# Optimization experiments

Measured on AMD Instinct MI355X. Metric: run time of the kernel, lower is better.

## Reference

```python
import jax, jax.numpy as jnp
import numpy as np

NUM_HEADS = 12
LOCAL_RATIO = 0.1


def setup_inputs() -> dict:
    key = jax.random.key(0)
    ks = jax.random.split(key, 8)
    B, N, C = 64, 785, 768
    x = jax.random.normal(ks[0], (B, N, C), dtype=jnp.float32)
    attention_rollout = jax.random.uniform(ks[1], (B, N, N), dtype=jnp.float32)
    s = 1.0 / np.sqrt(C)
    # Linear weights stored as [in, out] so y = x @ W + b (torch stores transposed)
    Wq = jax.random.normal(ks[2], (C, C), dtype=jnp.float32) * s
    bq = jax.random.normal(ks[3], (C,), dtype=jnp.float32) * 0.01
    Wkv = jax.random.normal(ks[4], (C, 2 * C), dtype=jnp.float32) * s
    bkv = jax.random.normal(ks[5], (2 * C,), dtype=jnp.float32) * 0.01
    Wp = jax.random.normal(ks[6], (C, C), dtype=jnp.float32) * s
    bp = jax.random.normal(ks[7], (C,), dtype=jnp.float32) * 0.01
    return {"x": x, "attention_rollout": attention_rollout, "Wq": Wq, "bq": bq,
            "Wkv": Wkv, "bkv": bkv, "Wp": Wp, "bp": bp}


def reference(x, attention_rollout, Wq, bq, Wkv, bkv, Wp, bp):
    B, N, C = x.shape
    H = NUM_HEADS
    D = C // H
    scale = D ** -0.5
    num_local = max(1, int(LOCAL_RATIO * (N - 1)))  # static

    # --- top-R% query selection from attention rollout (CLS row, skip CLS col) ---
    cls_attention = attention_rollout[:, 0, 1:]            # (B, N-1)
    _, top_idx = jax.lax.top_k(cls_attention, num_local)    # (B, L)
    local_indices = top_idx + 1                              # shift past CLS

    # gather selected queries: (B, L, C)
    local_queries = jnp.take_along_axis(x, local_indices[:, :, None], axis=1)

    # --- projections ---
    q = (local_queries @ Wq + bq).reshape(B, num_local, H, D).transpose(0, 2, 1, 3)  # (B,H,L,D)
    kv = (x @ Wkv + bkv).reshape(B, N, 2, H, D)
    k = kv[:, :, 0].transpose(0, 2, 1, 3)  # (B,H,N,D)
    v = kv[:, :, 1].transpose(0, 2, 1, 3)  # (B,H,N,D)

    # --- cross-attention: local queries attend to global keys/values ---
    attn = jax.nn.softmax(jnp.einsum('bhqd,bhkd->bhqk', q, k) * scale, axis=-1)
    local_out = jnp.einsum('bhqk,bhkd->bhqd', attn, v).transpose(0, 2, 1, 3).reshape(B, num_local, C)
    local_out = local_out @ Wp + bp

    # --- scatter back: selected rows get local_out, the rest keep x ---
    output = jax.vmap(lambda xb, ib, ob: xb.at[ib].set(ob))(x, local_indices, local_out)
    return output
```

## Files before the change

kernel.cpp:

```cpp
#include <hip/hip_runtime.h>

typedef short bfrag __attribute__((ext_vector_type(8)));
typedef float facc  __attribute__((ext_vector_type(4)));
typedef unsigned short usv4 __attribute__((ext_vector_type(4)));

#define MFMA_BF16(a,b,c) __builtin_amdgcn_mfma_f32_16x16x32_bf16((a),(b),(c),0,0,0)

__device__ __forceinline__ unsigned short f2bf(float f){
  unsigned int u = __float_as_uint(f);
  return (unsigned short)((u + 0x7FFFu + ((u >> 16) & 1u)) >> 16);
}

__global__ void wtrans_k(const float* __restrict__ W, unsigned short* __restrict__ Wt,
                         int K, int N){
  __shared__ float tile[32][33];
  int n0 = blockIdx.x * 32, k0 = blockIdx.y * 32;
  int tx = threadIdx.x, ty = threadIdx.y;
#pragma unroll
  for (int r = 0; r < 4; r++)
    tile[ty + r*8][tx] = W[(size_t)(k0 + ty + r*8) * N + n0 + tx];
  __syncthreads();
#pragma unroll
  for (int r = 0; r < 4; r++)
    Wt[(size_t)(n0 + ty + r*8) * K + k0 + tx] = f2bf(tile[tx][ty + r*8]);
}

__global__ void topk_k(const float* __restrict__ ar, int* __restrict__ lidx){
  int b = blockIdx.x, tid = threadIdx.x, w = tid >> 6, lane = tid & 63;
  __shared__ unsigned long long keys[784];
  __shared__ unsigned long long wred[4];
  const float* src = ar + (size_t)b * 785 * 785 + 1;
  for (int i = tid; i < 784; i += 256){
    unsigned int bits = __float_as_uint(src[i]);
    keys[i] = ((unsigned long long)bits << 32) | (unsigned int)(1023 - i);
  }
  __syncthreads();
  for (int t = 0; t < 78; t++){
    unsigned long long best = 0;
    for (int i = tid; i < 784; i += 256){ unsigned long long k = keys[i]; if (k > best) best = k; }
#pragma unroll
    for (int m = 1; m < 64; m <<= 1){
      unsigned long long o = __shfl_xor(best, m); if (o > best) best = o;
    }
    if (lane == 0) wred[w] = best;
    __syncthreads();
    if (tid == 0){
      unsigned long long bb = wred[0];
      for (int i = 1; i < 4; i++) if (wred[i] > bb) bb = wred[i];
      int idx = 1023 - (int)(bb & 0xFFFFFFFFull);
      lidx[b * 78 + t] = idx + 1;
      keys[idx] = 0;
    }
    __syncthreads();
  }
}

__global__ void cvt_k(const float* __restrict__ in, unsigned short* __restrict__ o){
  for (int i = blockIdx.x * 256 + threadIdx.x; i < 9646080; i += 2048 * 256){
    float4 v = ((const float4*)in)[i];
    usv4 u; u[0]=f2bf(v.x); u[1]=f2bf(v.y); u[2]=f2bf(v.z); u[3]=f2bf(v.w);
    ((usv4*)o)[i] = u;
  }
}

__global__ void copy_k(const float* __restrict__ in, float* __restrict__ o){
  for (int i = blockIdx.x * 256 + threadIdx.x; i < 9646080; i += 2048 * 256)
    ((float4*)o)[i] = ((const float4*)in)[i];
}

__global__ void gather_k(const float* __restrict__ x, const int* __restrict__ lidx,
                         unsigned short* __restrict__ Xq){
  int r = blockIdx.x;
  int b = r / 78;
  int n = lidx[r];
  float4 v = ((const float4*)(x + ((size_t)b * 785 + n) * 768))[threadIdx.x];
  usv4 u; u[0]=f2bf(v.x); u[1]=f2bf(v.y); u[2]=f2bf(v.z); u[3]=f2bf(v.w);
  ((usv4*)(Xq + (size_t)r * 768))[threadIdx.x] = u;
}

template<int MODE>
__global__ __launch_bounds__(256)
void gemm_k(const unsigned short* __restrict__ A, const unsigned short* __restrict__ Bt,
            const float* __restrict__ bias, unsigned short* __restrict__ O1,
            unsigned short* __restrict__ O2, float* __restrict__ Of,
            const int* __restrict__ lidx, int M)
{
  __shared__ unsigned short As[128 * 32];
  __shared__ unsigned short Bs[128 * 32];
  int nwg = gridDim.x * gridDim.y;
  int lin = blockIdx.x + blockIdx.y * gridDim.x;
  int q8 = nwg >> 3, r8 = nwg & 7, xcd = lin & 7, ii = lin >> 3;
  int wg = (xcd < r8 ? xcd * (q8 + 1) : r8 * (q8 + 1) + (xcd - r8) * q8) + ii;
  int ntile = wg % gridDim.x, mtile = wg / gridDim.x;
  int mbase = mtile * 128, nbase = ntile * 128;
  int tid = threadIdx.x, wid = tid >> 6, lane = tid & 63;
  int lr = lane & 15, lc = lane >> 4;
  int wm = wid >> 1, wn = wid & 1;

  facc z = {0.f, 0.f, 0.f, 0.f};
  facc acc[4][4];
#pragma unroll
  for (int a = 0; a < 4; a++)
#pragma unroll
    for (int b = 0; b < 4; b++) acc[a][b] = z;

  int a_off[4], b_off[4];
#pragma unroll
  for (int i = 0; i < 4; i++){
    int ra = wm * 64 + i * 16 + lr;
    a_off[i] = ra * 32 + ((lc ^ ((ra >> 1) & 3)) << 3);
    int rb = wn * 64 + i * 16 + lr;
    b_off[i] = rb * 32 + ((lc ^ ((rb >> 1) & 3)) << 3);
  }

  for (int kt = 0; kt < 24; kt++){
#pragma unroll
    for (int is = 0; is < 2; is++){
      int t = is * 256 + wid * 64 + lane;
      int row = t >> 2, ch = t & 3;
      int sc = (ch ^ ((row >> 1) & 3)) << 3;
      const unsigned short* ga = A  + (size_t)(mbase + row) * 768 + kt * 32 + sc;
      const unsigned short* gb = Bt + (size_t)(nbase + row) * 768 + kt * 32 + sc;
      __builtin_amdgcn_global_load_lds((const __attribute__((address_space(1))) unsigned int*)ga,
          (__attribute__((address_space(3))) unsigned int*)&As[(is * 256 + wid * 64) * 8], 16, 0, 0);
      __builtin_amdgcn_global_load_lds((const __attribute__((address_space(1))) unsigned int*)gb,
          (__attribute__((address_space(3))) unsigned int*)&Bs[(is * 256 + wid * 64) * 8], 16, 0, 0);
    }
    asm volatile("s_waitcnt vmcnt(0)" ::: "memory");
    __syncthreads();
    bfrag af[4], bfr[4];
#pragma unroll
    for (int i = 0; i < 4; i++){
      af[i]  = *(const bfrag*)&As[a_off[i]];
      bfr[i] = *(const bfrag*)&Bs[b_off[i]];
    }
#pragma unroll
    for (int mi = 0; mi < 4; mi++)
#pragma unroll
      for (int ni = 0; ni < 4; ni++)
        acc[mi][ni] = MFMA_BF16(af[mi], bfr[ni], acc[mi][ni]);
    __syncthreads();
  }

  int rbase = mbase + wm * 64, cbase = nbase + wn * 64;
#pragma unroll
  for (int mi = 0; mi < 4; mi++){
    int r0 = rbase + mi * 16 + lc * 4;
#pragma unroll
    for (int ni = 0; ni < 4; ni++){
      int c = cbase + ni * 16 + lr;
      float bv = bias[c];
#pragma unroll
      for (int j = 0; j < 4; j++){
        int r = r0 + j;
        if (r >= M) continue;
        float val = acc[mi][ni][j] + bv;
        if constexpr (MODE == 0){
          int b = r / 785, n = r - b * 785;
          if (c < 768){
            int hh = c >> 6, d = c & 63;
            O1[(((size_t)b * 12 + hh) * 800 + n) * 64 + d] = f2bf(val);
          } else {
            int c2 = c - 768, hh = c2 >> 6, d = c2 & 63;
            O2[(((size_t)b * 12 + hh) * 64 + d) * 800 + n] = f2bf(val);
          }
        } else if constexpr (MODE == 1){
          int b = r / 78, i2 = r - b * 78;
          int hh = c >> 6, d = c & 63;
          O1[(((size_t)b * 12 + hh) * 80 + i2) * 64 + d] = f2bf(val);
        } else {
          int b = r / 78;
          int n = lidx[r];
          Of[((size_t)b * 785 + n) * 768 + c] = val;
        }
      }
    }
  }
}

#define LOADKV(t, kf, vf) do { int kb_ = (t) * 32;                                        \
  _Pragma("unroll") for (int fj = 0; fj < 2; fj++)                                        \
  _Pragma("unroll") for (int kc = 0; kc < 2; kc++)                                        \
    kf[fj][kc] = *(const bfrag*)(Kb + (size_t)(kb_ + fj*16 + lr) * 64 + kc*32 + lc*8);    \
  _Pragma("unroll") for (int fd = 0; fd < 4; fd++)                                        \
    vf[fd] = *(const bfrag*)(Vb + (size_t)(fd*16 + lr) * 800 + kb_ + lc*8); } while(0)

__global__ __launch_bounds__(256)
void attn_k(const unsigned short* __restrict__ Qbf, const unsigned short* __restrict__ Kbf,
            const unsigned short* __restrict__ Vt, unsigned short* __restrict__ aout)
{
  int bh = blockIdx.x;
  int b = bh / 12, h = bh - b * 12;
  int tid = threadIdx.x, w = tid >> 6, l = tid & 63;
  int lr = l & 15, lc = l >> 4;
  __shared__ unsigned short P[4][80][40];
  __shared__ float Op[80][64];
  __shared__ float Lp[4][80];
  const unsigned short* Qb = Qbf + (size_t)bh * 80 * 64;
  const unsigned short* Kb = Kbf + (size_t)bh * 800 * 64;
  const unsigned short* Vb = Vt  + (size_t)bh * 64 * 800;

  bfrag qa[5][2];
#pragma unroll
  for (int fi = 0; fi < 5; fi++)
#pragma unroll
    for (int kc = 0; kc < 2; kc++)
      qa[fi][kc] = *(const bfrag*)(Qb + (size_t)(fi*16 + lr) * 64 + kc*32 + lc*8);

  facc z = {0.f, 0.f, 0.f, 0.f};
  facc o[5][4];
  facc lacc[5];
#pragma unroll
  for (int fi = 0; fi < 5; fi++){ lacc[fi] = z;
#pragma unroll
    for (int fd = 0; fd < 4; fd++) o[fi][fd] = z; }

  bfrag kcur[2][2], vcur[4], knxt[2][2], vnxt[4];
  LOADKV(w, kcur, vcur);
  for (int t = w; t < 25; t += 4){
    int tn = (t + 4 < 25) ? t + 4 : t;
    LOADKV(tn, knxt, vnxt);
    int kb = t * 32;
#pragma unroll
    for (int fi = 0; fi < 5; fi++){
      facc s0 = z, s1 = z;
      s0 = MFMA_BF16(qa[fi][0], kcur[0][0], s0);
      s0 = MFMA_BF16(qa[fi][1], kcur[0][1], s0);
      s1 = MFMA_BF16(qa[fi][0], kcur[1][0], s1);
      s1 = MFMA_BF16(qa[fi][1], kcur[1][1], s1);
      int k0 = kb + lr, k1 = kb + 16 + lr;
#pragma unroll
      for (int j = 0; j < 4; j++){
        float p0 = (k0 < 785) ? __expf(s0[j] * 0.125f) : 0.f;
        float p1 = (k1 < 785) ? __expf(s1[j] * 0.125f) : 0.f;
        lacc[fi][j] += p0 + p1;
        P[w][fi*16 + lc*4 + j][lr]      = f2bf(p0);
        P[w][fi*16 + lc*4 + j][16 + lr] = f2bf(p1);
      }
    }
#pragma unroll
    for (int fi = 0; fi < 5; fi++){
      bfrag pa = *(const bfrag*)&P[w][fi*16 + lr][lc*8];
#pragma unroll
      for (int fd = 0; fd < 4; fd++)
        o[fi][fd] = MFMA_BF16(pa, vcur[fd], o[fi][fd]);
    }
#pragma unroll
    for (int fj = 0; fj < 2; fj++)
#pragma unroll
      for (int kc = 0; kc < 2; kc++) kcur[fj][kc] = knxt[fj][kc];
#pragma unroll
    for (int fd = 0; fd < 4; fd++) vcur[fd] = vnxt[fd];
  }

#pragma unroll
  for (int fi = 0; fi < 5; fi++)
#pragma unroll
    for (int j = 0; j < 4; j++){
      float v = lacc[fi][j];
#pragma unroll
      for (int m = 1; m < 16; m <<= 1) v += __shfl_xor(v, m);
      if (lr == 0) Lp[w][fi*16 + lc*4 + j] = v;
    }
  for (int ww = 0; ww < 4; ww++){
    if (w == ww){
#pragma unroll
      for (int fi = 0; fi < 5; fi++)
#pragma unroll
        for (int fd = 0; fd < 4; fd++)
#pragma unroll
          for (int j = 0; j < 4; j++){
            int q = fi*16 + lc*4 + j, d = fd*16 + lr;
            if (ww == 0) Op[q][d] = o[fi][fd][j];
            else         Op[q][d] += o[fi][fd][j];
          }
    }
    __syncthreads();
  }
  for (int idx = tid; idx < 78 * 64; idx += 256){
    int q = idx >> 6, d = idx & 63;
    float L = Lp[0][q] + Lp[1][q] + Lp[2][q] + Lp[3][q];
    aout[(size_t)(b * 78 + q) * 768 + h * 64 + d] = f2bf(Op[q][d] / L);
  }
}

extern "C" void kernel_launch(void* const* d_in, const int* in_sizes, int n_in,
                              void* d_out, int out_size, void* d_ws, size_t ws_size,
                              hipStream_t stream)
{
  (void)in_sizes; (void)n_in; (void)out_size; (void)ws_size;
  const float* x   = (const float*)d_in[0];
  const float* ar  = (const float*)d_in[1];
  const float* Wq  = (const float*)d_in[2];
  const float* bq  = (const float*)d_in[3];
  const float* Wkv = (const float*)d_in[4];
  const float* bkv = (const float*)d_in[5];
  const float* Wp  = (const float*)d_in[6];
  const float* bp  = (const float*)d_in[7];
  float* out = (float*)d_out;

  char* ws = (char*)d_ws;
  size_t off = 0;
  auto alloc = [&](size_t bytes){ void* p = ws + off; off += (bytes + 255) & ~(size_t)255; return p; };
  unsigned short* WtQ  = (unsigned short*)alloc((size_t)768 * 768 * 2);
  unsigned short* WtKV = (unsigned short*)alloc((size_t)1536 * 768 * 2);
  unsigned short* WtP  = (unsigned short*)alloc((size_t)768 * 768 * 2);
  unsigned short* Xbf  = (unsigned short*)alloc((size_t)50304 * 768 * 2);
  unsigned short* Xq   = (unsigned short*)alloc((size_t)4992 * 768 * 2);
  unsigned short* Qbf  = (unsigned short*)alloc((size_t)768 * 80 * 64 * 2);
  unsigned short* Kbf  = (unsigned short*)alloc((size_t)768 * 800 * 64 * 2);
  unsigned short* Vt   = (unsigned short*)alloc((size_t)768 * 64 * 800 * 2);
  unsigned short* Aout = (unsigned short*)alloc((size_t)4992 * 768 * 2);
  int* lidx = (int*)alloc((size_t)4992 * 4);

  wtrans_k<<<dim3(768/32, 768/32),  dim3(32, 8), 0, stream>>>(Wq,  WtQ,  768, 768);
  wtrans_k<<<dim3(1536/32, 768/32), dim3(32, 8), 0, stream>>>(Wkv, WtKV, 768, 1536);
  wtrans_k<<<dim3(768/32, 768/32),  dim3(32, 8), 0, stream>>>(Wp,  WtP,  768, 768);
  topk_k<<<64, 256, 0, stream>>>(ar, lidx);
  cvt_k<<<2048, 256, 0, stream>>>(x, Xbf);
  gather_k<<<4992, 192, 0, stream>>>(x, lidx, Xq);
  gemm_k<0><<<dim3(12, 393), 256, 0, stream>>>(Xbf, WtKV, bkv, Kbf, Vt, nullptr, nullptr, 50240);
  gemm_k<1><<<dim3(6, 39),   256, 0, stream>>>(Xq,  WtQ,  bq,  Qbf, nullptr, nullptr, nullptr, 4992);
  attn_k<<<768, 256, 0, stream>>>(Qbf, Kbf, Vt, Aout);
  copy_k<<<2048, 256, 0, stream>>>(x, out);
  gemm_k<2><<<dim3(6, 39),   256, 0, stream>>>(Aout, WtP, bp, nullptr, nullptr, out, lidx, 4992);
}
```

Baseline: 808.3 us.

## Add dedicated 256x256 KV GEMM, fuse convert+copy, wave-level topk, MFMA priority

Replaces the generic KV projection GEMM with a 512-thread kernel that uses 256x256 tiles, K-step 64, double-buffered direct global-to-LDS loads and an XOR-swizzled LDS layout. This targets the dominant projection cost through more data reuse and overlap of loads with MFMA. Several other changes ride along. The bf16 conversion and the output copy of x become one pass. Top-k runs in a single wavefront with keys held in registers instead of shared memory and block barriers. The attention kernel raises wave priority around its MFMA sections. The larger tiles read past row 50240, so the Xbf buffer is padded to cover it.

```diff
diff --git a/kernel.cpp b/kernel.cpp
--- a/kernel.cpp
+++ b/kernel.cpp
@@ -26,46 +26,37 @@
 }
 
 __global__ void topk_k(const float* __restrict__ ar, int* __restrict__ lidx){
-  int b = blockIdx.x, tid = threadIdx.x, w = tid >> 6, lane = tid & 63;
-  __shared__ unsigned long long keys[784];
-  __shared__ unsigned long long wred[4];
+  int b = blockIdx.x, l = threadIdx.x;
   const float* src = ar + (size_t)b * 785 * 785 + 1;
-  for (int i = tid; i < 784; i += 256){
-    unsigned int bits = __float_as_uint(src[i]);
-    keys[i] = ((unsigned long long)bits << 32) | (unsigned int)(1023 - i);
-  }
-  __syncthreads();
+  unsigned long long key[13];
+#pragma unroll
+  for (int j = 0; j < 13; j++){
+    int i = l + 64 * j;
+    unsigned int bits = (i < 784) ? __float_as_uint(src[i]) : 0u;
+    key[j] = ((unsigned long long)bits << 32) | (unsigned int)(1023 - i);
+  }
   for (int t = 0; t < 78; t++){
     unsigned long long best = 0;
-    for (int i = tid; i < 784; i += 256){ unsigned long long k = keys[i]; if (k > best) best = k; }
+#pragma unroll
+    for (int j = 0; j < 13; j++) if (key[j] > best) best = key[j];
 #pragma unroll
     for (int m = 1; m < 64; m <<= 1){
       unsigned long long o = __shfl_xor(best, m); if (o > best) best = o;
     }
-    if (lane == 0) wred[w] = best;
-    __syncthreads();
-    if (tid == 0){
-      unsigned long long bb = wred[0];
-      for (int i = 1; i < 4; i++) if (wred[i] > bb) bb = wred[i];
-      int idx = 1023 - (int)(bb & 0xFFFFFFFFull);
-      lidx[b * 78 + t] = idx + 1;
-      keys[idx] = 0;
-    }
-    __syncthreads();
-  }
-}
-
-__global__ void cvt_k(const float* __restrict__ in, unsigned short* __restrict__ o){
+    if (l == 0) lidx[b * 78 + t] = 1024 - (int)(best & 0xFFFFFFFFull);
+#pragma unroll
+    for (int j = 0; j < 13; j++) if (key[j] == best) key[j] = 0;
+  }
+}
+
+__global__ void cvtcopy_k(const float* __restrict__ in, float* __restrict__ o,
+                          unsigned short* __restrict__ xb){
   for (int i = blockIdx.x * 256 + threadIdx.x; i < 9646080; i += 2048 * 256){
     float4 v = ((const float4*)in)[i];
+    ((float4*)o)[i] = v;
     usv4 u; u[0]=f2bf(v.x); u[1]=f2bf(v.y); u[2]=f2bf(v.z); u[3]=f2bf(v.w);
-    ((usv4*)o)[i] = u;
-  }
-}
-
-__global__ void copy_k(const float* __restrict__ in, float* __restrict__ o){
-  for (int i = blockIdx.x * 256 + threadIdx.x; i < 9646080; i += 2048 * 256)
-    ((float4*)o)[i] = ((const float4*)in)[i];
+    ((usv4*)xb)[i] = u;
+  }
 }
 
 __global__ void gather_k(const float* __restrict__ x, const int* __restrict__ lidx,
@@ -78,12 +69,117 @@
   ((usv4*)(Xq + (size_t)r * 768))[threadIdx.x] = u;
 }
 
+__global__ __launch_bounds__(512, 2)
+void gemm_kv(const unsigned short* __restrict__ A, const unsigned short* __restrict__ Bt,
+             const float* __restrict__ bias, unsigned short* __restrict__ Kout,
+             unsigned short* __restrict__ Vout)
+{
+  __shared__ unsigned short As[2][16384];
+  __shared__ unsigned short Bs[2][16384];
+  int gx = gridDim.x;
+  int nwg = gx * gridDim.y;
+  int lin = blockIdx.x + blockIdx.y * gx;
+  int q8 = nwg >> 3, r8 = nwg & 7, xcd = lin & 7, ii = lin >> 3;
+  int wg = (xcd < r8 ? xcd * (q8 + 1) : r8 * (q8 + 1) + (xcd - r8) * q8) + ii;
+  int ntile = wg % gx, mtile = wg / gx;
+  int mbase = mtile * 256, nbase = ntile * 256;
+  int tid = threadIdx.x, wid = tid >> 6, lane = tid & 63;
+  int lr = lane & 15, lc = lane >> 4;
+  int wm = wid >> 2, wn = wid & 3;
+
+  int trow = tid >> 3;
+  int tchunk = (tid & 7) ^ (trow & 7);
+  const unsigned short* gA = A  + (size_t)(mbase + trow) * 768 + tchunk * 8;
+  const unsigned short* gB = Bt + (size_t)(nbase + trow) * 768 + tchunk * 8;
+
+#define STAGE(bufi, kt) do {                                                              \
+  _Pragma("unroll") for (int i_ = 0; i_ < 4; i_++){                                       \
+    __builtin_amdgcn_global_load_lds(                                                     \
+      (const __attribute__((address_space(1))) unsigned int*)(gA + (size_t)i_*49152 + (kt)*64), \
+      (__attribute__((address_space(3))) unsigned int*)&As[bufi][i_*4096 + wid*512], 16, 0, 0); \
+    __builtin_amdgcn_global_load_lds(                                                     \
+      (const __attribute__((address_space(1))) unsigned int*)(gB + (size_t)i_*49152 + (kt)*64), \
+      (__attribute__((address_space(3))) unsigned int*)&Bs[bufi][i_*4096 + wid*512], 16, 0, 0); \
+  } } while(0)
+
+  facc z = {0.f, 0.f, 0.f, 0.f};
+  facc acc[8][4];
+#pragma unroll
+  for (int a = 0; a < 8; a++)
+#pragma unroll
+    for (int b = 0; b < 4; b++) acc[a][b] = z;
+
+  int s0 = lc ^ (lr & 7);
+
+  STAGE(0, 0);
+  for (int kt = 0; kt < 12; ++kt){
+    int cur = kt & 1;
+    if (kt < 11){
+      STAGE(cur ^ 1, kt + 1);
+      asm volatile("s_waitcnt vmcnt(8)" ::: "memory");
+    } else {
+      asm volatile("s_waitcnt vmcnt(0)" ::: "memory");
+    }
+    __builtin_amdgcn_s_barrier();
+    __builtin_amdgcn_sched_barrier(0);
+    asm volatile("" ::: "memory");
+    const unsigned short* Ab = As[cur];
+    const unsigned short* Bb = Bs[cur];
+#pragma unroll
+    for (int kk = 0; kk < 2; kk++){
+      bfrag af[8], bf[4];
+      int so = (s0 ^ (kk << 2)) << 3;
+#pragma unroll
+      for (int mf = 0; mf < 8; mf++)
+        af[mf] = *(const bfrag*)&Ab[(wm*128 + mf*16 + lr) * 64 + so];
+#pragma unroll
+      for (int nf = 0; nf < 4; nf++)
+        bf[nf] = *(const bfrag*)&Bb[(wn*64 + nf*16 + lr) * 64 + so];
+      __builtin_amdgcn_s_setprio(1);
+#pragma unroll
+      for (int mf = 0; mf < 8; mf++)
+#pragma unroll
+        for (int nf = 0; nf < 4; nf++)
+          acc[mf][nf] = MFMA_BF16(af[mf], bf[nf], acc[mf][nf]);
+      __builtin_amdgcn_s_setprio(0);
+    }
+    asm volatile("" ::: "memory");
+    __builtin_amdgcn_sched_barrier(0);
+    __builtin_amdgcn_s_barrier();
+  }
+
+  int cblk = ntile * 4 + wn;
+  int hh = (cblk < 12) ? cblk : cblk - 12;
+  const float* bp2 = bias + cblk * 64;
+  int rb = mbase + wm * 128;
+#pragma unroll
+  for (int mf = 0; mf < 8; mf++){
+    int r0 = rb + mf * 16 + lc * 4;
+#pragma unroll
+    for (int nf = 0; nf < 4; nf++){
+      int d = nf * 16 + lr;
+      float bv = bp2[d];
+#pragma unroll
+      for (int j = 0; j < 4; j++){
+        int r = r0 + j;
+        if (r >= 50240) continue;
+        float val = acc[mf][nf][j] + bv;
+        int b = r / 785, n = r - b * 785;
+        if (cblk < 12)
+          Kout[(((size_t)b * 12 + hh) * 800 + n) * 64 + d] = f2bf(val);
+        else
+          Vout[(((size_t)b * 12 + hh) * 64 + d) * 800 + n] = f2bf(val);
+      }
+    }
+  }
+#undef STAGE
+}
+
 template<int MODE>
 __global__ __launch_bounds__(256)
 void gemm_k(const unsigned short* __restrict__ A, const unsigned short* __restrict__ Bt,
             const float* __restrict__ bias, unsigned short* __restrict__ O1,
-            unsigned short* __restrict__ O2, float* __restrict__ Of,
-            const int* __restrict__ lidx, int M)
+            float* __restrict__ Of, const int* __restrict__ lidx, int M)
 {
   __shared__ unsigned short As[128 * 32];
   __shared__ unsigned short Bs[128 * 32];
@@ -155,16 +251,7 @@
         int r = r0 + j;
         if (r >= M) continue;
         float val = acc[mi][ni][j] + bv;
-        if constexpr (MODE == 0){
-          int b = r / 785, n = r - b * 785;
-          if (c < 768){
-            int hh = c >> 6, d = c & 63;
-            O1[(((size_t)b * 12 + hh) * 800 + n) * 64 + d] = f2bf(val);
-          } else {
-            int c2 = c - 768, hh = c2 >> 6, d = c2 & 63;
-            O2[(((size_t)b * 12 + hh) * 64 + d) * 800 + n] = f2bf(val);
-          }
-        } else if constexpr (MODE == 1){
+        if constexpr (MODE == 1){
           int b = r / 78, i2 = r - b * 78;
           int hh = c >> 6, d = c & 63;
           O1[(((size_t)b * 12 + hh) * 80 + i2) * 64 + d] = f2bf(val);
@@ -221,6 +308,7 @@
     int tn = (t + 4 < 25) ? t + 4 : t;
     LOADKV(tn, knxt, vnxt);
     int kb = t * 32;
+    __builtin_amdgcn_s_setprio(1);
 #pragma unroll
     for (int fi = 0; fi < 5; fi++){
       facc s0 = z, s1 = z;
@@ -228,6 +316,7 @@
       s0 = MFMA_BF16(qa[fi][1], kcur[0][1], s0);
       s1 = MFMA_BF16(qa[fi][0], kcur[1][0], s1);
       s1 = MFMA_BF16(qa[fi][1], kcur[1][1], s1);
+      __builtin_amdgcn_s_setprio(0);
       int k0 = kb + lr, k1 = kb + 16 + lr;
 #pragma unroll
       for (int j = 0; j < 4; j++){
@@ -237,6 +326,7 @@
         P[w][fi*16 + lc*4 + j][lr]      = f2bf(p0);
         P[w][fi*16 + lc*4 + j][16 + lr] = f2bf(p1);
       }
+      __builtin_amdgcn_s_setprio(1);
     }
 #pragma unroll
     for (int fi = 0; fi < 5; fi++){
@@ -245,6 +335,7 @@
       for (int fd = 0; fd < 4; fd++)
         o[fi][fd] = MFMA_BF16(pa, vcur[fd], o[fi][fd]);
     }
+    __builtin_amdgcn_s_setprio(0);
 #pragma unroll
     for (int fj = 0; fj < 2; fj++)
 #pragma unroll
@@ -305,7 +396,7 @@
   unsigned short* WtQ  = (unsigned short*)alloc((size_t)768 * 768 * 2);
   unsigned short* WtKV = (unsigned short*)alloc((size_t)1536 * 768 * 2);
   unsigned short* WtP  = (unsigned short*)alloc((size_t)768 * 768 * 2);
-  unsigned short* Xbf  = (unsigned short*)alloc((size_t)50304 * 768 * 2);
+  unsigned short* Xbf  = (unsigned short*)alloc((size_t)50432 * 768 * 2);
   unsigned short* Xq   = (unsigned short*)alloc((size_t)4992 * 768 * 2);
   unsigned short* Qbf  = (unsigned short*)alloc((size_t)768 * 80 * 64 * 2);
   unsigned short* Kbf  = (unsigned short*)alloc((size_t)768 * 800 * 64 * 2);
@@ -316,12 +407,11 @@
   wtrans_k<<<dim3(768/32, 768/32),  dim3(32, 8), 0, stream>>>(Wq,  WtQ,  768, 768);
   wtrans_k<<<dim3(1536/32, 768/32), dim3(32, 8), 0, stream>>>(Wkv, WtKV, 768, 1536);
   wtrans_k<<<dim3(768/32, 768/32),  dim3(32, 8), 0, stream>>>(Wp,  WtP,  768, 768);
-  topk_k<<<64, 256, 0, stream>>>(ar, lidx);
-  cvt_k<<<2048, 256, 0, stream>>>(x, Xbf);
+  topk_k<<<64, 64, 0, stream>>>(ar, lidx);
+  cvtcopy_k<<<2048, 256, 0, stream>>>(x, out, Xbf);
   gather_k<<<4992, 192, 0, stream>>>(x, lidx, Xq);
-  gemm_k<0><<<dim3(12, 393), 256, 0, stream>>>(Xbf, WtKV, bkv, Kbf, Vt, nullptr, nullptr, 50240);
-  gemm_k<1><<<dim3(6, 39),   256, 0, stream>>>(Xq,  WtQ,  bq,  Qbf, nullptr, nullptr, nullptr, 4992);
+  gemm_kv<<<dim3(6, 197), 512, 0, stream>>>(Xbf, WtKV, bkv, Kbf, Vt);
+  gemm_k<1><<<dim3(6, 39), 256, 0, stream>>>(Xq,  WtQ,  bq,  Qbf, nullptr, nullptr, 4992);
   attn_k<<<768, 256, 0, stream>>>(Qbf, Kbf, Vt, Aout);
-  copy_k<<<2048, 256, 0, stream>>>(x, out);
-  gemm_k<2><<<dim3(6, 39),   256, 0, stream>>>(Aout, WtP, bp, nullptr, nullptr, out, lidx, 4992);
-}
+  gemm_k<2><<<dim3(6, 39), 256, 0, stream>>>(Aout, WtP, bp, nullptr, out, lidx, 4992);
+}
```

Measured after the change: 833.1 us. +3.1%, slower.
